# Performance work log

Hardware: AMD Instinct MI355X
Metric: run time of the kernel (lower is better)

The kernel has to match this reference:

```python
import jax, jax.numpy as jnp
import numpy as np

B, S, E = 8, 4096, 128
H, O = 64, 64  # attention_hidden_dim, out_dim


def setup_inputs() -> dict:
    key = jax.random.key(0)
    ks = jax.random.split(key, 4)
    x = jax.random.normal(ks[0], (B, S, E), dtype=jnp.float32)
    Wq = jax.random.normal(ks[1], (E, H), dtype=jnp.float32) * (1.0 / np.sqrt(E))
    Wk = jax.random.normal(ks[2], (E, H), dtype=jnp.float32) * (1.0 / np.sqrt(E))
    Wv = jax.random.normal(ks[3], (E, O), dtype=jnp.float32) * (1.0 / np.sqrt(E))
    bq = jnp.zeros((H,), dtype=jnp.float32)
    bk = jnp.zeros((H,), dtype=jnp.float32)
    bv = jnp.zeros((O,), dtype=jnp.float32)
    return {"x": x, "Wq": Wq, "bq": bq, "Wk": Wk, "bk": bk, "Wv": Wv, "bv": bv}


def reference(x, Wq, bq, Wk, bk, Wv, bv):
    # Batched version of the per-sample loop: q = x@Wq+bq, etc.
    q = jnp.einsum("bse,eh->bsh", x, Wq) + bq   # [B,S,H]
    k = jnp.einsum("bse,eh->bsh", x, Wk) + bk   # [B,S,H]
    v = jnp.einsum("bse,eo->bso", x, Wv) + bv   # [B,S,O]
    scores = jnp.einsum("bqh,bkh->bqk", q, k)   # QK^T per sample, [B,S,S]
    attn = jax.nn.softmax(scores, axis=-1)       # softmax over key dim
    out = jnp.einsum("bqk,bko->bqo", attn, v)   # [B,S,O]
    return out
```

## Files before the change

### kernel.cpp

```cpp
#include <hip/hip_runtime.h>
#include <math.h>

#define BB 8
#define SS 4096
#define EE 128
#define HH 64
#define NT 16
#define LOG2E 1.44269504088896f

typedef _Float16 f16;
typedef __attribute__((ext_vector_type(8))) _Float16 f16x8;
typedef __attribute__((ext_vector_type(4))) float f32x4;
typedef __attribute__((ext_vector_type(16))) float f32x16;
typedef __attribute__((ext_vector_type(4))) unsigned int u32x4;

__device__ __forceinline__ unsigned int pk2h(float a, float b) {
    return __builtin_bit_cast(unsigned int, __builtin_amdgcn_cvt_pkrtz(a, b));
}

__device__ __forceinline__ void async_copy16(void* lds, const void* g) {
    __builtin_amdgcn_global_load_lds(
        (const __attribute__((address_space(1))) void*)g,
        (__attribute__((address_space(3))) void*)lds, 16, 0, 0);
}

__device__ __forceinline__ void vm_barrier() {
    asm volatile("s_waitcnt vmcnt(0) lgkmcnt(0)" ::: "memory");
    __builtin_amdgcn_s_barrier();
    __builtin_amdgcn_sched_barrier(0);
}

__global__ __launch_bounds__(256) void wtrans_kernel(
    const float* __restrict__ Wq, const float* __restrict__ Wk,
    const float* __restrict__ Wv, f16* __restrict__ Wt)
{
    const int idx = blockIdx.x * 256 + threadIdx.x;
    if (idx >= 192 * 128) return;
    const int col = idx >> 7, e = idx & 127;
    const float v = (col < 64)  ? Wq[e * 64 + col] * LOG2E
                  : (col < 128) ? Wk[e * 64 + (col - 64)]
                                : Wv[e * 64 + (col - 128)];
    Wt[col * 128 + e] = (f16)v;
}

__global__ __launch_bounds__(256) void qkv_kernel(
    const float* __restrict__ x, const f16* __restrict__ Wt,
    const float* __restrict__ bq, const float* __restrict__ bk,
    const float* __restrict__ bv,
    f16* __restrict__ Q, f16* __restrict__ K, f16* __restrict__ Vt)
{
    const int tid  = threadIdx.x;
    const int lane = tid & 63;
    const int wid  = tid >> 6;
    const int ln15 = lane & 15;
    const int lg   = lane >> 4;
    const long rowbase = (long)blockIdx.x * 64;

    f16x8 xa[4];
    {
        const float* xp = x + (rowbase + wid * 16 + ln15) * EE + lg * 8;
#pragma unroll
        for (int s = 0; s < 4; ++s) {
            const float4 u = *(const float4*)(xp + s * 32);
            const float4 v = *(const float4*)(xp + s * 32 + 4);
            const u32x4 w = {pk2h(u.x, u.y), pk2h(u.z, u.w),
                             pk2h(v.x, v.y), pk2h(v.z, v.w)};
            xa[s] = __builtin_bit_cast(f16x8, w);
        }
    }

    f32x4 acc[12];
#pragma unroll
    for (int ct = 0; ct < 12; ++ct) acc[ct] = (f32x4){0.f, 0.f, 0.f, 0.f};

#pragma unroll
    for (int ct = 0; ct < 12; ++ct) {
        const f16* wtp = Wt + (ct * 16 + ln15) * 128 + lg * 8;
#pragma unroll
        for (int s = 0; s < 4; ++s) {
            const f16x8 wb = *(const f16x8*)(wtp + s * 32);
            acc[ct] = __builtin_amdgcn_mfma_f32_16x16x32_f16(xa[s], wb, acc[ct], 0, 0, 0);
        }
    }

    const long grow0 = rowbase + wid * 16 + 4 * lg;
#pragma unroll
    for (int ct = 0; ct < 4; ++ct) {
        const int col = ct * 16 + ln15;
        const float b = bq[col] * LOG2E;
#pragma unroll
        for (int r = 0; r < 4; ++r)
            Q[(grow0 + r) * HH + col] = (f16)(acc[ct][r] + b);
    }
#pragma unroll
    for (int ct = 4; ct < 8; ++ct) {
        const int col = (ct - 4) * 16 + ln15;
        const float b = bk[col];
#pragma unroll
        for (int r = 0; r < 4; ++r)
            K[(grow0 + r) * HH + col] = (f16)(acc[ct][r] + b);
    }
    {
        const long batch = rowbase >> 12;
        const long inrow0 = (rowbase & 4095) + wid * 16;
        const long inrowP = inrow0 + 8 * (lg & 1) + 4 * (lg >> 1);
#pragma unroll
        for (int ct = 8; ct < 12; ++ct) {
            const int o = (ct - 8) * 16 + ln15;
            const float b = bv[o];
            unsigned long long pk =
                (unsigned long long)pk2h(acc[ct][0] + b, acc[ct][1] + b) |
                ((unsigned long long)pk2h(acc[ct][2] + b, acc[ct][3] + b) << 32);
            *(unsigned long long*)(Vt + ((long)batch * HH + o) * SS + inrowP) = pk;
        }
    }
}

__global__ __launch_bounds__(256, 4) void flash_kernel(
    const f16* __restrict__ Q, const f16* __restrict__ K,
    const f16* __restrict__ Vt, f16* __restrict__ Onorm,
    float* __restrict__ lse)
{
    __shared__ __align__(16) short k_s[2][64 * HH];
    __shared__ __align__(16) short v_s[2][64 * HH];

    const int tid  = threadIdx.x;
    const int lane = tid & 63;
    const int wid  = tid >> 6;
    const int q31  = lane & 31;
    const int h5   = lane >> 5;
    const int batch = blockIdx.x & 7;
    const int split = (blockIdx.x >> 3) & 3;
    const int qblk  = blockIdx.x >> 5;
    const int k0base = split * (SS / 4);

    f16x8 qf[4];
    {
        const long qrow = (long)batch * SS + qblk * 128 + wid * 32 + q31;
        const f16* qp = Q + qrow * HH + 8 * h5;
        qf[0] = *(const f16x8*)(qp);
        qf[1] = *(const f16x8*)(qp + 16);
        qf[2] = *(const f16x8*)(qp + 32);
        qf[3] = *(const f16x8*)(qp + 48);
    }

    f32x16 oacc0 = {0.f,0.f,0.f,0.f,0.f,0.f,0.f,0.f,0.f,0.f,0.f,0.f,0.f,0.f,0.f,0.f};
    f32x16 oacc1 = oacc0;
    float m = -1e30f, l = 0.f;

    const int crow = lane >> 3;
    const int ccs  = ((lane & 7) * 16) ^ (crow << 4);
    const int row0 = wid * 16 + crow;
    const char* kgb = (const char*)(K + ((long)batch * SS + k0base) * HH);
    const char* vgb = (const char*)(Vt + (long)batch * HH * SS);
    const long koff = (long)row0 * 128 + ccs;
    const long voff = (long)row0 * (SS * 2) + k0base * 2 + ccs;

    auto issue = [&](int t, int b) __attribute__((always_inline)) {
        char* kl = (char*)k_s[b] + wid * 2048;
        char* vl = (char*)v_s[b] + wid * 2048;
        const char* kg = kgb + (long)t * (64 * 128) + koff;
        const char* vg = vgb + (long)t * 128 + voff;
        async_copy16(kl,        kg);
        async_copy16(kl + 1024, kg + 1024);
        async_copy16(vl,        vg);
        async_copy16(vl + 1024, vg + 8 * (SS * 2));
    };

    auto compute = [&](int cur) __attribute__((always_inline)) {
        const char* ks = (const char*)k_s[cur];
        const char* vs = (const char*)v_s[cur];

        f32x16 s0 = {0.f,0.f,0.f,0.f,0.f,0.f,0.f,0.f,0.f,0.f,0.f,0.f,0.f,0.f,0.f,0.f};
        f32x16 s1 = s0;
        __builtin_amdgcn_s_setprio(1);
#pragma unroll
        for (int step = 0; step < 4; ++step) {
            const int cb = step * 32 + 16 * h5;
            const int r0 = q31;
            const f16x8 ka0 = *(const f16x8*)(ks + ((r0 * 128 + cb) ^ ((r0 & 7) << 4)));
            s0 = __builtin_amdgcn_mfma_f32_32x32x16_f16(ka0, qf[step], s0, 0, 0, 0);
            const int r1 = q31 + 32;
            const f16x8 ka1 = *(const f16x8*)(ks + ((r1 * 128 + cb) ^ ((r1 & 7) << 4)));
            s1 = __builtin_amdgcn_mfma_f32_32x32x16_f16(ka1, qf[step], s1, 0, 0, 0);
        }
        __builtin_amdgcn_s_setprio(0);

        float tm = s0[0];
#pragma unroll
        for (int i = 1; i < 16; ++i) tm = fmaxf(tm, s0[i]);
#pragma unroll
        for (int i = 0; i < 16; ++i) tm = fmaxf(tm, s1[i]);
        tm = fmaxf(tm, __shfl_xor(tm, 32));
        if (!__all(tm <= m + 11.5f)) {
            const float mn = fmaxf(m, tm);
            const float alpha = __builtin_amdgcn_exp2f(m - mn);
            l *= alpha;
            oacc0 *= alpha;
            oacc1 *= alpha;
            m = mn;
        }

        unsigned int pk[16];
        float ps = 0.f;
#pragma unroll
        for (int i = 0; i < 8; ++i) {
            const float a = __builtin_amdgcn_exp2f(s0[2 * i] - m);
            const float b = __builtin_amdgcn_exp2f(s0[2 * i + 1] - m);
            ps += a + b;
            pk[i] = pk2h(a, b);
        }
#pragma unroll
        for (int i = 0; i < 8; ++i) {
            const float a = __builtin_amdgcn_exp2f(s1[2 * i] - m);
            const float b = __builtin_amdgcn_exp2f(s1[2 * i + 1] - m);
            ps += a + b;
            pk[8 + i] = pk2h(a, b);
        }
        ps += __shfl_xor(ps, 32);
        l += ps;

        __builtin_amdgcn_s_setprio(1);
#pragma unroll
        for (int mb = 0; mb < 4; ++mb) {
            const u32x4 pw = {pk[4 * mb], pk[4 * mb + 1], pk[4 * mb + 2], pk[4 * mb + 3]};
            const f16x8 pb = __builtin_bit_cast(f16x8, pw);
            const int cb = 32 * mb + 16 * h5;
#pragma unroll
            for (int oh = 0; oh < 2; ++oh) {
                const int row = q31 + 32 * oh;
                const f16x8 va = *(const f16x8*)(vs + ((row * 128 + cb) ^ ((row & 7) << 4)));
                if (oh == 0)
                    oacc0 = __builtin_amdgcn_mfma_f32_32x32x16_f16(va, pb, oacc0, 0, 0, 0);
                else
                    oacc1 = __builtin_amdgcn_mfma_f32_32x32x16_f16(va, pb, oacc1, 0, 0, 0);
            }
        }
        __builtin_amdgcn_s_setprio(0);
    };

    issue(0, 0);
    vm_barrier();

    for (int t = 0; t < NT; t += 2) {
        issue(t + 1, 1);
        compute(0);
        vm_barrier();
        if (t + 2 < NT) issue(t + 2, 0);
        compute(1);
        vm_barrier();
    }

    const float linv = 1.0f / l;
    const long tok = (long)split * (BB * SS) + (long)batch * SS + qblk * 128 + wid * 32 + q31;
    f16* ob = Onorm + tok * HH;
#pragma unroll
    for (int i = 0; i < 16; ++i) {
        const int od = (i & 3) + 8 * (i >> 2) + 4 * h5;
        ob[od]      = (f16)(oacc0[i] * linv);
        ob[od + 32] = (f16)(oacc1[i] * linv);
    }
    if (h5 == 0)
        lse[tok] = m + __builtin_amdgcn_logf(l);
}

__global__ __launch_bounds__(256) void merge_kernel(
    const f16* __restrict__ Onorm, const float* __restrict__ lse,
    float* __restrict__ Out)
{
    const int gid = blockIdx.x * 256 + threadIdx.x;
    const long row = gid >> 3;
    const int c0 = (gid & 7) * 8;
    const long NR = (long)BB * SS;

    float ls[4];
#pragma unroll
    for (int i = 0; i < 4; ++i) ls[i] = lse[i * NR + row];
    const float M = fmaxf(fmaxf(ls[0], ls[1]), fmaxf(ls[2], ls[3]));
    float g[4], denom = 0.f;
#pragma unroll
    for (int i = 0; i < 4; ++i) { g[i] = __builtin_amdgcn_exp2f(ls[i] - M); denom += g[i]; }
    const float inv = 1.0f / denom;

    float acc[8];
#pragma unroll
    for (int j = 0; j < 8; ++j) acc[j] = 0.f;
#pragma unroll
    for (int i = 0; i < 4; ++i) {
        const f16x8 o = *(const f16x8*)(Onorm + (i * NR + row) * HH + c0);
#pragma unroll
        for (int j = 0; j < 8; ++j) acc[j] = fmaf(g[i], (float)o[j], acc[j]);
    }
    float4 r0, r1;
    r0.x = acc[0] * inv; r0.y = acc[1] * inv; r0.z = acc[2] * inv; r0.w = acc[3] * inv;
    r1.x = acc[4] * inv; r1.y = acc[5] * inv; r1.z = acc[6] * inv; r1.w = acc[7] * inv;
    float4* dst = (float4*)(Out + row * HH + c0);
    dst[0] = r0;
    dst[1] = r1;
}

extern "C" void kernel_launch(void* const* d_in, const int* in_sizes, int n_in,
                              void* d_out, int out_size, void* d_ws, size_t ws_size,
                              hipStream_t stream) {
    const float* x  = (const float*)d_in[0];
    const float* Wq = (const float*)d_in[1];
    const float* bq = (const float*)d_in[2];
    const float* Wk = (const float*)d_in[3];
    const float* bk = (const float*)d_in[4];
    const float* Wv = (const float*)d_in[5];
    const float* bv = (const float*)d_in[6];
    float* out = (float*)d_out;

    const size_t NTOK = (size_t)BB * SS;
    f16* Q  = (f16*)d_ws;
    f16* K  = Q + NTOK * HH;
    f16* Vt = K + NTOK * HH;
    f16* Wt = Vt + NTOK * HH;
    f16* Onorm = Wt + 192 * 128;
    float* lse = (float*)(Onorm + 4 * NTOK * HH);

    wtrans_kernel<<<96, 256, 0, stream>>>(Wq, Wk, Wv, Wt);
    qkv_kernel<<<BB * SS / 64, 256, 0, stream>>>(x, Wt, bq, bk, bv, Q, K, Vt);
    flash_kernel<<<BB * 4 * (SS / 128), 256, 0, stream>>>(Q, K, Vt, Onorm, lse);
    merge_kernel<<<BB * SS * 8 / 256, 256, 0, stream>>>(Onorm, lse, out);
}
```

Measured before the change: 78.11 us.

## Software-pipeline QK^T of next tile with softmax-PV of current tile

Splits K and V async loads into separate issues and splits per-tile compute into a QK^T stage and a softmax+PV stage. The loop now computes scores for tile t+1 while doing softmax and PV for tile t, with K loaded one tile ahead of V. This is meant to let MFMA work overlap the exp/max VALU work. The row max is also computed as a tree reduction to shorten the dependency chain. In exchange it holds two sets of score accumulators, which raises register pressure, and LDS buffer reuse timing becomes harder to reason about.

```diff
diff --git a/kernel.cpp b/kernel.cpp
--- a/kernel.cpp
+++ b/kernel.cpp
@@ -156,23 +156,24 @@
     const long koff = (long)row0 * 128 + ccs;
     const long voff = (long)row0 * (SS * 2) + k0base * 2 + ccs;
 
-    auto issue = [&](int t, int b) __attribute__((always_inline)) {
+    auto issue_k = [&](int t, int b) __attribute__((always_inline)) {
         char* kl = (char*)k_s[b] + wid * 2048;
-        char* vl = (char*)v_s[b] + wid * 2048;
         const char* kg = kgb + (long)t * (64 * 128) + koff;
-        const char* vg = vgb + (long)t * 128 + voff;
         async_copy16(kl,        kg);
         async_copy16(kl + 1024, kg + 1024);
+    };
+    auto issue_v = [&](int t, int b) __attribute__((always_inline)) {
+        char* vl = (char*)v_s[b] + wid * 2048;
+        const char* vg = vgb + (long)t * 128 + voff;
         async_copy16(vl,        vg);
         async_copy16(vl + 1024, vg + 8 * (SS * 2));
     };
 
-    auto compute = [&](int cur) __attribute__((always_inline)) {
-        const char* ks = (const char*)k_s[cur];
-        const char* vs = (const char*)v_s[cur];
-
-        f32x16 s0 = {0.f,0.f,0.f,0.f,0.f,0.f,0.f,0.f,0.f,0.f,0.f,0.f,0.f,0.f,0.f,0.f};
-        f32x16 s1 = s0;
+    auto qkt = [&](const short* ksp, f32x16& s0, f32x16& s1)
+        __attribute__((always_inline)) {
+        const char* ks = (const char*)ksp;
+        s0 = (f32x16){0.f,0.f,0.f,0.f,0.f,0.f,0.f,0.f,0.f,0.f,0.f,0.f,0.f,0.f,0.f,0.f};
+        s1 = s0;
         __builtin_amdgcn_s_setprio(1);
 #pragma unroll
         for (int step = 0; step < 4; ++step) {
@@ -185,12 +186,26 @@
             s1 = __builtin_amdgcn_mfma_f32_32x32x16_f16(ka1, qf[step], s1, 0, 0, 0);
         }
         __builtin_amdgcn_s_setprio(0);
-
-        float tm = s0[0];
-#pragma unroll
-        for (int i = 1; i < 16; ++i) tm = fmaxf(tm, s0[i]);
-#pragma unroll
-        for (int i = 0; i < 16; ++i) tm = fmaxf(tm, s1[i]);
+    };
+
+    auto smpv = [&](f32x16& s0, f32x16& s1, const short* vsp)
+        __attribute__((always_inline)) {
+        const char* vs = (const char*)vsp;
+        float c0 = fmaxf(fmaxf(s0[0], s0[1]), s0[2]);
+        c0 = fmaxf(fmaxf(c0, s0[3]), s0[4]);
+        c0 = fmaxf(fmaxf(c0, s0[5]), s0[6]);
+        float c1 = fmaxf(fmaxf(s0[8], s0[9]), s0[10]);
+        c1 = fmaxf(fmaxf(c1, s0[11]), s0[12]);
+        c1 = fmaxf(fmaxf(c1, s0[13]), s0[14]);
+        float c2 = fmaxf(fmaxf(s1[0], s1[1]), s1[2]);
+        c2 = fmaxf(fmaxf(c2, s1[3]), s1[4]);
+        c2 = fmaxf(fmaxf(c2, s1[5]), s1[6]);
+        float c3 = fmaxf(fmaxf(s1[8], s1[9]), s1[10]);
+        c3 = fmaxf(fmaxf(c3, s1[11]), s1[12]);
+        c3 = fmaxf(fmaxf(c3, s1[13]), s1[14]);
+        c0 = fmaxf(fmaxf(c0, s0[7]), s0[15]);
+        c2 = fmaxf(fmaxf(c2, s1[7]), s1[15]);
+        float tm = fmaxf(fmaxf(c0, c1), fmaxf(c2, c3));
         tm = fmaxf(tm, __shfl_xor(tm, 32));
         if (!__all(tm <= m + 11.5f)) {
             const float mn = fmaxf(m, tm);
@@ -239,15 +254,25 @@
         __builtin_amdgcn_s_setprio(0);
     };
 
-    issue(0, 0);
+    f32x16 sA0, sA1, sB0, sB1;
+
+    issue_k(0, 0);
+    issue_v(0, 0);
     vm_barrier();
+    issue_k(1, 1);
+    qkt(k_s[0], sA0, sA1);
+    vm_barrier();
 
     for (int t = 0; t < NT; t += 2) {
-        issue(t + 1, 1);
-        compute(0);
+        if (t + 2 < NT) issue_k(t + 2, 0);
+        issue_v(t + 1, 1);
+        qkt(k_s[1], sB0, sB1);
+        smpv(sA0, sA1, v_s[0]);
         vm_barrier();
-        if (t + 2 < NT) issue(t + 2, 0);
-        compute(1);
+        if (t + 3 < NT) issue_k(t + 3, 1);
+        if (t + 2 < NT) issue_v(t + 2, 0);
+        if (t + 2 < NT) qkt(k_s[0], sA0, sA1);
+        smpv(sB0, sB1, v_s[1]);
         vm_barrier();
     }
 
```

Result: slower. 109.3 us (+40.0%).
